# Kernel tuning notes

Hardware: AMD Instinct MI355X
Metric: run time of the kernel (lower is better)

## Reference

```python
import jax, jax.numpy as jnp
import numpy as np

V_SIZES = [2562, 10242, 40962]
E_SIZES = [7680, 30720, 122880]
NG = 8000


def _chamfer(a, b):
    # a: [Na,3], b: [Nb,3] -> squared NN distances (dist_a:[Na], dist_b:[Nb])
    # ||a-b||^2 = ||a||^2 + ||b||^2 - 2 a.b  (GEMM form, same math as pairwise diff)
    an = jnp.sum(a * a, axis=-1)
    bn = jnp.sum(b * b, axis=-1)
    d = an[:, None] + bn[None, :] - 2.0 * (a @ b.T)  # [Na,Nb]
    d = jnp.maximum(d, 0.0)
    return d.min(axis=1), d.min(axis=0)


def _edge_regularization(pred, edges):
    # nn.MSELoss(reduction='none') over endpoint pairs, mean, scaled by coord dim
    diff = pred[edges[:, 0]] - pred[edges[:, 1]]  # [E,3]
    return jnp.mean(diff * diff) * pred.shape[-1]


def _laplace_coord(x, lap_idx):
    # x: [N,3]; lap_idx: [N,10] -> cols 0..7 neighbor idx (-1 pad), col 9 count
    nbr = lap_idx[:, :8]
    valid = nbr >= 0
    idx = jnp.where(valid, nbr, 0)
    v = x[idx]                                  # [N,8,3]
    v = jnp.where(valid[..., None], v, 0.0)
    cnt = lap_idx[:, -1].astype(x.dtype)
    return x - v.sum(axis=1) / cnt[:, None]


def _laplace_regularization(feats, pts, lap_idx):
    lap1 = _laplace_coord(feats, lap_idx)
    lap2 = _laplace_coord(pts, lap_idx)
    d = lap1 - lap2
    return jnp.mean(d * d) * lap1.shape[-1]


def _p2m_loss(pred_pts, pred_feats, gt, edges, lap_idx):
    lap_const = [0.2, 1.0, 1.0]
    chamfer_loss = 0.0
    edge_loss = 0.0
    lap_loss = 0.0
    for i in range(3):
        d1, d2 = _chamfer(gt, pred_pts[i])
        chamfer_loss = chamfer_loss + jnp.mean(d1) + jnp.mean(d2)
        edge_loss = edge_loss + _edge_regularization(pred_pts[i], edges[i])
        lap_loss = lap_loss + lap_const[i] * _laplace_regularization(pred_feats[i], pred_pts[i], lap_idx[i])
    loss = 100.0 * chamfer_loss + 0.1 * edge_loss + 0.3 * lap_loss
    return loss, chamfer_loss, edge_loss, lap_loss


def _make_lap_idx(key, V):
    k1, k2 = jax.random.split(key)
    nbr = jax.random.randint(k1, (V, 8), 0, V)
    mask = jax.random.uniform(k2, (V, 8)) < 0.8
    mask = mask.at[:, 0].set(True)  # at least one valid neighbor
    nbr = jnp.where(mask, nbr, -1)
    cnt = mask.sum(axis=1)
    dummy = jnp.zeros((V, 1), jnp.int32)
    return jnp.concatenate([nbr, dummy, cnt[:, None]], axis=1).astype(jnp.int32)


def setup_inputs() -> dict:
    key = jax.random.key(0)
    ks = jax.random.split(key, 16)
    inp = {}
    for i, V in enumerate(V_SIZES):
        inp[f"pred_pts_{i+1}"] = jax.random.normal(ks[i], (V, 3), dtype=jnp.float32)
        inp[f"pred_feats_{i+1}"] = jax.random.normal(ks[3 + i], (V, 3), dtype=jnp.float32)
        inp[f"edges_{i+1}"] = jax.random.randint(ks[6 + i], (E_SIZES[i], 2), 0, V).astype(jnp.int32)
        inp[f"lap_idx_{i+1}"] = _make_lap_idx(ks[9 + i], V)
    inp["gt_pts"] = jax.random.normal(ks[12], (1, NG, 3), dtype=jnp.float32)
    return inp


def reference(pred_pts_1, pred_pts_2, pred_pts_3,
              pred_feats_1, pred_feats_2, pred_feats_3,
              gt_pts,
              edges_1, edges_2, edges_3,
              lap_idx_1, lap_idx_2, lap_idx_3):
    gt = gt_pts.reshape(-1, 3)
    return _p2m_loss(
        [pred_pts_1, pred_pts_2, pred_pts_3],
        [pred_feats_1, pred_feats_2, pred_feats_3],
        gt,
        [edges_1, edges_2, edges_3],
        [lap_idx_1, lap_idx_2, lap_idx_3],
    )
```

## Files before the change

### kernel.cpp

```cpp
#include <hip/hip_runtime.h>

#define NG 8000
#define V1 2562
#define V2 10242
#define V3 40962
#define E1 7680
#define E2 30720
#define E3 122880
#define NPRED (V1 + V2 + V3)
#define ND1   (3 * NG)
#define NMIN  (ND1 + NPRED)
#define ABATCH 16
#define MAXCHUNK 512

struct PassTab {
    int NA[6], NB[6], h[6], xb[6], chunk[6], ooff[6], base[7];
};

__device__ __forceinline__ double block_reduce_add(double v, double* sm) {
    int lane = threadIdx.x & 63;
    int wid  = threadIdx.x >> 6;
    for (int off = 32; off > 0; off >>= 1) v += __shfl_down(v, off, 64);
    if (lane == 0) sm[wid] = v;
    __syncthreads();
    double r = 0.0;
    if (wid == 0) {
        int nw = blockDim.x >> 6;
        r = (lane < nw) ? sm[lane] : 0.0;
        for (int off = 32; off > 0; off >>= 1) r += __shfl_down(r, off, 64);
    }
    return r;
}

__global__ void k_init(unsigned int* __restrict__ mins, double* __restrict__ acc) {
    int i = blockIdx.x * blockDim.x + threadIdx.x;
    if (i < 8) acc[i] = 0.0;
    int stride = gridDim.x * blockDim.x;
    for (int k = i; k < NMIN; k += stride) mins[k] = 0x7f800000u;
}

__launch_bounds__(256)
__global__ void k_pair_all(const float* __restrict__ gt,
                           const float* __restrict__ q1,
                           const float* __restrict__ q2,
                           const float* __restrict__ q3,
                           unsigned int* __restrict__ mins, PassTab T) {
    __shared__ float4 sb[MAXCHUNK];
    int bid = blockIdx.x, tid = threadIdx.x;

    int p = 0;
    while (p < 5 && bid >= T.base[p + 1]) ++p;
    int rel  = bid - T.base[p];
    int xb   = T.xb[p];
    int xblk = rel % xb, yblk = rel / xb;
    int NA = T.NA[p], NB = T.NB[p], h = T.h[p], chunk = T.chunk[p];
    int pi = (p < 3) ? p : p - 3;
    const float* pr = (pi == 0) ? q1 : ((pi == 1) ? q2 : q3);
    const float* A  = (p < 3) ? gt : pr;
    const float* B  = (p < 3) ? pr : gt;

    int j0 = yblk * chunk;
    int cnt = min(NB - j0, chunk);
    for (int i = tid; i < cnt; i += 256) {
        int j = 3 * (j0 + i);
        float x = B[j], y = B[j + 1], z = B[j + 2];
        sb[i] = make_float4(x, y, z, fmaf(x, x, fmaf(y, y, z * z)));
    }
    __syncthreads();

    int t = xblk * 256 + tid;
    if (t >= h) return;

    float nx[ABATCH], ny_[ABATCH], nz[ABATCH], aw[ABATCH], m[ABATCH];
#pragma unroll
    for (int q = 0; q < ABATCH; ++q) {
        int tq = t + q * h; if (tq > NA - 1) tq = NA - 1;
        int j = 3 * tq;
        float x = A[j], y = A[j + 1], z = A[j + 2];
        nx[q] = -2.f * x; ny_[q] = -2.f * y; nz[q] = -2.f * z;
        aw[q] = fmaf(x, x, fmaf(y, y, z * z));
        m[q] = __builtin_inff();
    }

#define DOT(q, bb) fmaf(nz[q], bb.z, fmaf(ny_[q], bb.y, fmaf(nx[q], bb.x, bb.w)))
    int k = 0;
    for (; k + 2 <= cnt; k += 2) {
        float4 b0 = sb[k], b1 = sb[k + 1];
#pragma unroll
        for (int q = 0; q < ABATCH; ++q) {
            float d0 = DOT(q, b0), d1 = DOT(q, b1);
            m[q] = fminf(fminf(m[q], d0), d1);
        }
    }
    if (k < cnt) {
        float4 b = sb[k];
#pragma unroll
        for (int q = 0; q < ABATCH; ++q) m[q] = fminf(m[q], DOT(q, b));
    }
#undef DOT

    unsigned int* out = mins + T.ooff[p];
#pragma unroll
    for (int q = 0; q < ABATCH; ++q) {
        int tq = t + q * h;
        if (tq < NA) atomicMin(out + tq, __float_as_uint(fmaxf(aw[q] + m[q], 0.f)));
    }
}

#define R0 NMIN
#define R1 (E1 + E2 + E3)
#define R2 NPRED
__global__ void k_post(const unsigned int* __restrict__ mins,
                       const float* __restrict__ p1, const float* __restrict__ p2,
                       const float* __restrict__ p3,
                       const int* __restrict__ e1, const int* __restrict__ e2,
                       const int* __restrict__ e3,
                       const float* __restrict__ f1, const float* __restrict__ f2,
                       const float* __restrict__ f3,
                       const int* __restrict__ l1, const int* __restrict__ l2,
                       const int* __restrict__ l3,
                       double* __restrict__ acc) {
    __shared__ double sm[8];
    double s0 = 0.0, s1 = 0.0, s2 = 0.0;
    int stride = gridDim.x * blockDim.x;
    int gid = blockIdx.x * blockDim.x + threadIdx.x;
    for (int i = gid; i < R0 + R1 + R2; i += stride) {
        if (i < R0) {
            double w;
            if (i < ND1) w = 1.0 / NG;
            else {
                int t = i - ND1;
                w = (t < V1) ? (1.0 / V1) : ((t < V1 + V2) ? (1.0 / V2) : (1.0 / V3));
            }
            s0 += (double)__uint_as_float(mins[i]) * w;
        } else if (i < R0 + R1) {
            int q = i - R0;
            const float* p; const int* e; int k; double w;
            if (q < E1)            { p = p1; e = e1; k = q;            w = 1.0 / E1; }
            else if (q < E1 + E2)  { p = p2; e = e2; k = q - E1;       w = 1.0 / E2; }
            else                   { p = p3; e = e3; k = q - E1 - E2;  w = 1.0 / E3; }
            int u = e[2 * k], v = e[2 * k + 1];
            float dx = p[3 * u]     - p[3 * v];
            float dy = p[3 * u + 1] - p[3 * v + 1];
            float dz = p[3 * u + 2] - p[3 * v + 2];
            s1 += w * (double)(dx * dx + dy * dy + dz * dz);
        } else {
            int q = i - R0 - R1;
            const float* f; const float* p; const int* l; int k; double w;
            if (q < V1)            { f = f1; p = p1; l = l1; k = q;            w = 0.2 / V1; }
            else if (q < V1 + V2)  { f = f2; p = p2; l = l2; k = q - V1;       w = 1.0 / V2; }
            else                   { f = f3; p = p3; l = l3; k = q - V1 - V2;  w = 1.0 / V3; }
            const int* row = l + 10 * k;
            float sfx = 0.f, sfy = 0.f, sfz = 0.f, spx = 0.f, spy = 0.f, spz = 0.f;
#pragma unroll
            for (int r = 0; r < 8; ++r) {
                int n = row[r];
                if (n >= 0) {
                    sfx += f[3 * n]; sfy += f[3 * n + 1]; sfz += f[3 * n + 2];
                    spx += p[3 * n]; spy += p[3 * n + 1]; spz += p[3 * n + 2];
                }
            }
            float inv = 1.0f / (float)row[9];
            float dx = (f[3 * k]     - p[3 * k])     - (sfx - spx) * inv;
            float dy = (f[3 * k + 1] - p[3 * k + 1]) - (sfy - spy) * inv;
            float dz = (f[3 * k + 2] - p[3 * k + 2]) - (sfz - spz) * inv;
            s2 += w * (double)(dx * dx + dy * dy + dz * dz);
        }
    }
    double r0 = block_reduce_add(s0, sm); __syncthreads();
    double r1 = block_reduce_add(s1, sm); __syncthreads();
    double r2 = block_reduce_add(s2, sm);
    if (threadIdx.x == 0) {
        atomicAdd(acc + 0, r0);
        atomicAdd(acc + 1, r1);
        atomicAdd(acc + 2, r2);
    }
}

__global__ void k_final(const double* __restrict__ acc, float* __restrict__ out) {
    if (threadIdx.x == 0 && blockIdx.x == 0) {
        double ch = acc[0], ed = acc[1], lp = acc[2];
        out[0] = (float)(100.0 * ch + 0.1 * ed + 0.3 * lp);
        out[1] = (float)ch;
        out[2] = (float)ed;
        out[3] = (float)lp;
    }
}

static void build_tab(PassTab& T) {
    const int NAs[6]  = { NG, NG, NG, V1, V2, V3 };
    const int NBs[6]  = { V1, V2, V3, NG, NG, NG };
    const int ooff[6] = { 0, NG, 2 * NG, ND1, ND1 + V1, ND1 + V1 + V2 };
    const double totalPairs = 2.0 * ((double)NG * NPRED);
    const int TARGET_BLOCKS = 1024;
    int base = 0;
    for (int p = 0; p < 6; ++p) {
        int NA = NAs[p], NB = NBs[p];
        int h  = (NA + ABATCH - 1) / ABATCH;
        int xb = (h + 255) / 256;
        double share = ((double)NA * NB) / totalPairs;
        int ny = (int)(share * TARGET_BLOCKS / xb + 0.5);
        int nyMin = (NB + MAXCHUNK - 1) / MAXCHUNK;
        int nyMax = NB / 128;
        if (nyMax < nyMin) nyMax = nyMin;
        if (ny < nyMin) ny = nyMin;
        if (ny > nyMax) ny = nyMax;
        int chunk = (NB + ny - 1) / ny;
        ny = (NB + chunk - 1) / chunk;
        T.NA[p] = NA; T.NB[p] = NB; T.h[p] = h; T.xb[p] = xb;
        T.chunk[p] = chunk; T.ooff[p] = ooff[p]; T.base[p] = base;
        base += xb * ny;
    }
    T.base[6] = base;
}

extern "C" void kernel_launch(void* const* d_in, const int* in_sizes, int n_in,
                              void* d_out, int out_size, void* d_ws, size_t ws_size,
                              hipStream_t stream) {
    const float *pp[3], *pf[3], *gt;
    const int *ed[3], *li[3];
    if (in_sizes[1] == 3 * V1) {
        pp[0] = (const float*)d_in[0];  pf[0] = (const float*)d_in[1];
        ed[0] = (const int*)d_in[2];    li[0] = (const int*)d_in[3];
        pp[1] = (const float*)d_in[4];  pf[1] = (const float*)d_in[5];
        ed[1] = (const int*)d_in[6];    li[1] = (const int*)d_in[7];
        pp[2] = (const float*)d_in[8];  pf[2] = (const float*)d_in[9];
        ed[2] = (const int*)d_in[10];   li[2] = (const int*)d_in[11];
        gt = (const float*)d_in[12];
    } else {
        pp[0] = (const float*)d_in[0];  pp[1] = (const float*)d_in[1];  pp[2] = (const float*)d_in[2];
        pf[0] = (const float*)d_in[3];  pf[1] = (const float*)d_in[4];  pf[2] = (const float*)d_in[5];
        gt    = (const float*)d_in[6];
        ed[0] = (const int*)d_in[7];    ed[1] = (const int*)d_in[8];    ed[2] = (const int*)d_in[9];
        li[0] = (const int*)d_in[10];   li[1] = (const int*)d_in[11];   li[2] = (const int*)d_in[12];
    }

    PassTab T;
    build_tab(T);

    char* ws = (char*)d_ws;
    double*       acc  = (double*)ws;
    unsigned int* mins = (unsigned int*)(ws + 64);

    k_init<<<160, 256, 0, stream>>>(mins, acc);
    k_pair_all<<<T.base[6], 256, 0, stream>>>(gt, pp[0], pp[1], pp[2], mins, T);
    k_post<<<256, 256, 0, stream>>>(mins, pp[0], pp[1], pp[2],
                                    ed[0], ed[1], ed[2],
                                    pf[0], pf[1], pf[2],
                                    li[0], li[1], li[2], acc);
    k_final<<<1, 64, 0, stream>>>(acc, (float*)d_out);
}
```

Before: 171.0 us.

## Compute chamfer pairwise distances with bf16 split-precision MFMA matrix ops

```diff
diff --git a/kernel.cpp b/kernel.cpp
--- a/kernel.cpp
+++ b/kernel.cpp
@@ -8,14 +8,34 @@
 #define E2 30720
 #define E3 122880
 #define NPRED (V1 + V2 + V3)
+#define NPK   (NG + NPRED)
 #define ND1   (3 * NG)
 #define NMIN  (ND1 + NPRED)
-#define ABATCH 16
-#define MAXCHUNK 512
-
-struct PassTab {
-    int NA[6], NB[6], h[6], xb[6], chunk[6], ooff[6], base[7];
-};
+#define CHUNK 512
+#define AAW   128
+#define ABLK  512
+
+typedef __attribute__((ext_vector_type(8))) short bf16x8;
+typedef __attribute__((ext_vector_type(4))) float f32x4;
+
+struct PassTab { int NA[6], NB[6], Aoff[6], Boff[6], ooff[6], xb[6], base[7]; };
+
+__device__ __forceinline__ float min3f(float a, float b, float c) {
+    float r;
+    asm("v_min3_f32 %0, %1, %2, %3" : "=v"(r) : "v"(a), "v"(b), "v"(c));
+    return r;
+}
+
+__device__ __forceinline__ unsigned short f2bf(float f) {
+    unsigned int u = __float_as_uint(f);
+    return (unsigned short)((u + 0x7fffu + ((u >> 16) & 1u)) >> 16);
+}
+__device__ __forceinline__ float bf2f(unsigned short b) {
+    return __uint_as_float(((unsigned int)b) << 16);
+}
+__device__ __forceinline__ unsigned int pk(unsigned short lo, unsigned short hi) {
+    return (unsigned int)lo | ((unsigned int)hi << 16);
+}
 
 __device__ __forceinline__ double block_reduce_add(double v, double* sm) {
     int lane = threadIdx.x & 63;
@@ -32,20 +52,52 @@
     return r;
 }
 
-__global__ void k_init(unsigned int* __restrict__ mins, double* __restrict__ acc) {
-    int i = blockIdx.x * blockDim.x + threadIdx.x;
-    if (i < 8) acc[i] = 0.0;
+__global__ void k_prep(const float* __restrict__ gt,
+                       const float* __restrict__ q1, const float* __restrict__ q2,
+                       const float* __restrict__ q3,
+                       uint4* __restrict__ Arec, uint4* __restrict__ Brec,
+                       float* __restrict__ an, unsigned int* __restrict__ mins,
+                       double* __restrict__ acc) {
     int stride = gridDim.x * blockDim.x;
-    for (int k = i; k < NMIN; k += stride) mins[k] = 0x7f800000u;
+    for (int i = blockIdx.x * blockDim.x + threadIdx.x; i < NMIN; i += stride) {
+        if (i < 8) acc[i] = 0.0;
+        mins[i] = 0x7f800000u;
+        if (i < NPK) {
+            const float* src; int k;
+            if (i < NG) { src = gt; k = i; }
+            else {
+                int t = i - NG;
+                if (t < V1)            { src = q1; k = t; }
+                else if (t < V1 + V2)  { src = q2; k = t - V1; }
+                else                   { src = q3; k = t - V1 - V2; }
+            }
+            float x = src[3 * k], y = src[3 * k + 1], z = src[3 * k + 2];
+            unsigned short hx = f2bf(x), hy = f2bf(y), hz = f2bf(z);
+            float hxf = bf2f(hx), hyf = bf2f(hy), hzf = bf2f(hz);
+            unsigned short lx = f2bf(x - hxf), ly = f2bf(y - hyf), lz = f2bf(z - hzf);
+            float bn = fmaf(x, x, fmaf(y, y, z * z));
+            unsigned short bnh = f2bf(bn);
+            unsigned short bnl = f2bf(bn - bf2f(bnh));
+            unsigned short nhx = f2bf(-2.f * hxf), nhy = f2bf(-2.f * hyf), nhz = f2bf(-2.f * hzf);
+            unsigned short nlx = f2bf(-2.f * bf2f(lx)), nly = f2bf(-2.f * bf2f(ly)), nlz = f2bf(-2.f * bf2f(lz));
+            size_t p = (size_t)i;
+            Arec[p * 4 + 0] = make_uint4(pk(nhx, nhy), pk(nhz, nhx), pk(nhy, nhz), pk(0x3F80, 0x3F80));
+            Arec[p * 4 + 1] = make_uint4(pk(nlx, nly), pk(nlz, 0), 0u, 0u);
+            Arec[p * 4 + 2] = make_uint4(0u, 0u, 0u, 0u);
+            Arec[p * 4 + 3] = make_uint4(0u, 0u, 0u, 0u);
+            Brec[p * 2 + 0] = make_uint4(pk(hx, hy), pk(hz, lx), pk(ly, lz), pk(bnh, bnl));
+            Brec[p * 2 + 1] = make_uint4(pk(hx, hy), pk(hz, 0), 0u, 0u);
+            an[i] = bn;
+        }
+    }
 }
 
 __launch_bounds__(256)
-__global__ void k_pair_all(const float* __restrict__ gt,
-                           const float* __restrict__ q1,
-                           const float* __restrict__ q2,
-                           const float* __restrict__ q3,
-                           unsigned int* __restrict__ mins, PassTab T) {
-    __shared__ float4 sb[MAXCHUNK];
+__global__ void k_pair_mfma(const uint4* __restrict__ Arec,
+                            const uint4* __restrict__ Brec,
+                            const float* __restrict__ an,
+                            unsigned int* __restrict__ mins, PassTab T) {
+    __shared__ uint4 sb[2 * CHUNK];
     int bid = blockIdx.x, tid = threadIdx.x;
 
     int p = 0;
@@ -53,57 +105,66 @@
     int rel  = bid - T.base[p];
     int xb   = T.xb[p];
     int xblk = rel % xb, yblk = rel / xb;
-    int NA = T.NA[p], NB = T.NB[p], h = T.h[p], chunk = T.chunk[p];
-    int pi = (p < 3) ? p : p - 3;
-    const float* pr = (pi == 0) ? q1 : ((pi == 1) ? q2 : q3);
-    const float* A  = (p < 3) ? gt : pr;
-    const float* B  = (p < 3) ? pr : gt;
-
-    int j0 = yblk * chunk;
-    int cnt = min(NB - j0, chunk);
-    for (int i = tid; i < cnt; i += 256) {
-        int j = 3 * (j0 + i);
-        float x = B[j], y = B[j + 1], z = B[j + 2];
-        sb[i] = make_float4(x, y, z, fmaf(x, x, fmaf(y, y, z * z)));
+    int NA = T.NA[p], NB = T.NB[p];
+    int Aoff = T.Aoff[p], Boff = T.Boff[p], ooff = T.ooff[p];
+
+    int j0  = yblk * CHUNK;
+    int cnt = min(NB - j0, CHUNK);
+
+    for (int i = tid; i < 2 * CHUNK; i += 256) {
+        int pt = i >> 1, gg = i & 1;
+        uint4 v;
+        if (pt < cnt) v = Brec[(size_t)(Boff + j0 + pt) * 2 + gg];
+        else          v = gg ? make_uint4(0u, 0u, 0u, 0u)
+                             : make_uint4(0u, 0u, 0u, 0x00007F80u);
+        sb[i] = v;
     }
     __syncthreads();
 
-    int t = xblk * 256 + tid;
-    if (t >= h) return;
-
-    float nx[ABATCH], ny_[ABATCH], nz[ABATCH], aw[ABATCH], m[ABATCH];
+    int l = tid & 63, w = tid >> 6;
+    int g = l >> 4, c = l & 15;
+    int Abase = xblk * ABLK + w * AAW;
+
+    union U { uint4 u; bf16x8 b; };
+
+    bf16x8 af[8];
+    float  m[8];
 #pragma unroll
-    for (int q = 0; q < ABATCH; ++q) {
-        int tq = t + q * h; if (tq > NA - 1) tq = NA - 1;
-        int j = 3 * tq;
-        float x = A[j], y = A[j + 1], z = A[j + 2];
-        nx[q] = -2.f * x; ny_[q] = -2.f * y; nz[q] = -2.f * z;
-        aw[q] = fmaf(x, x, fmaf(y, y, z * z));
-        m[q] = __builtin_inff();
-    }
-
-#define DOT(q, bb) fmaf(nz[q], bb.z, fmaf(ny_[q], bb.y, fmaf(nx[q], bb.x, bb.w)))
-    int k = 0;
-    for (; k + 2 <= cnt; k += 2) {
-        float4 b0 = sb[k], b1 = sb[k + 1];
+    for (int tt = 0; tt < 8; ++tt) {
+        int apt = Abase + tt * 16 + c;
+        int ap  = min(apt, NA - 1);
+        U u; u.u = Arec[(size_t)(Aoff + ap) * 4 + g];
+        af[tt] = u.b;
+        m[tt]  = __builtin_inff();
+    }
+
+    unsigned int msk = (g < 2) ? 0xFFFFFFFFu : 0u;
+    const uint4* bbase = sb + (c * 2 + (g & 1));
+    f32x4 zero = {0.f, 0.f, 0.f, 0.f};
+
+    for (int jb = 0; jb < cnt; jb += 16) {
+        uint4 r = bbase[jb * 2];
+        r.x &= msk; r.y &= msk; r.z &= msk; r.w &= msk;
+        U u; u.u = r;
+        bf16x8 bfr = u.b;
 #pragma unroll
-        for (int q = 0; q < ABATCH; ++q) {
-            float d0 = DOT(q, b0), d1 = DOT(q, b1);
-            m[q] = fminf(fminf(m[q], d0), d1);
+        for (int tt = 0; tt < 8; ++tt) {
+            f32x4 a = __builtin_amdgcn_mfma_f32_16x16x32_bf16(bfr, af[tt], zero, 0, 0, 0);
+            float t0 = min3f(a[0], a[1], a[2]);
+            m[tt] = min3f(m[tt], t0, a[3]);
         }
     }
-    if (k < cnt) {
-        float4 b = sb[k];
+
 #pragma unroll
-        for (int q = 0; q < ABATCH; ++q) m[q] = fminf(m[q], DOT(q, b));
-    }
-#undef DOT
-
-    unsigned int* out = mins + T.ooff[p];
-#pragma unroll
-    for (int q = 0; q < ABATCH; ++q) {
-        int tq = t + q * h;
-        if (tq < NA) atomicMin(out + tq, __float_as_uint(fmaxf(aw[q] + m[q], 0.f)));
+    for (int tt = 0; tt < 8; ++tt) {
+        float mm = m[tt];
+        mm = fminf(mm, __shfl_xor(mm, 16, 64));
+        mm = fminf(mm, __shfl_xor(mm, 32, 64));
+        int apt = Abase + tt * 16 + c;
+        if (g == 0 && apt < NA) {
+            float d = fmaxf(an[Aoff + apt] + mm, 0.f);
+            atomicMin(mins + ooff + apt, __float_as_uint(d));
+        }
     }
 }
 
@@ -190,25 +251,16 @@
 static void build_tab(PassTab& T) {
     const int NAs[6]  = { NG, NG, NG, V1, V2, V3 };
     const int NBs[6]  = { V1, V2, V3, NG, NG, NG };
-    const int ooff[6] = { 0, NG, 2 * NG, ND1, ND1 + V1, ND1 + V1 + V2 };
-    const double totalPairs = 2.0 * ((double)NG * NPRED);
-    const int TARGET_BLOCKS = 1024;
+    const int AoP[6]  = { 0, 0, 0, NG, NG + V1, NG + V1 + V2 };
+    const int BoP[6]  = { NG, NG + V1, NG + V1 + V2, 0, 0, 0 };
+    const int ooP[6]  = { 0, NG, 2 * NG, ND1, ND1 + V1, ND1 + V1 + V2 };
     int base = 0;
     for (int p = 0; p < 6; ++p) {
-        int NA = NAs[p], NB = NBs[p];
-        int h  = (NA + ABATCH - 1) / ABATCH;
-        int xb = (h + 255) / 256;
-        double share = ((double)NA * NB) / totalPairs;
-        int ny = (int)(share * TARGET_BLOCKS / xb + 0.5);
-        int nyMin = (NB + MAXCHUNK - 1) / MAXCHUNK;
-        int nyMax = NB / 128;
-        if (nyMax < nyMin) nyMax = nyMin;
-        if (ny < nyMin) ny = nyMin;
-        if (ny > nyMax) ny = nyMax;
-        int chunk = (NB + ny - 1) / ny;
-        ny = (NB + chunk - 1) / chunk;
-        T.NA[p] = NA; T.NB[p] = NB; T.h[p] = h; T.xb[p] = xb;
-        T.chunk[p] = chunk; T.ooff[p] = ooff[p]; T.base[p] = base;
+        int xb = (NAs[p] + ABLK - 1) / ABLK;
+        int ny = (NBs[p] + CHUNK - 1) / CHUNK;
+        T.NA[p] = NAs[p]; T.NB[p] = NBs[p];
+        T.Aoff[p] = AoP[p]; T.Boff[p] = BoP[p]; T.ooff[p] = ooP[p];
+        T.xb[p] = xb; T.base[p] = base;
         base += xb * ny;
     }
     T.base[6] = base;
@@ -240,10 +292,13 @@
 
     char* ws = (char*)d_ws;
     double*       acc  = (double*)ws;
-    unsigned int* mins = (unsigned int*)(ws + 64);
-
-    k_init<<<160, 256, 0, stream>>>(mins, acc);
-    k_pair_all<<<T.base[6], 256, 0, stream>>>(gt, pp[0], pp[1], pp[2], mins, T);
+    unsigned int* mins = (unsigned int*)(ws + 1024);
+    float*        an   = (float*)(ws + 400 * 1024);
+    uint4*        Arec = (uint4*)(ws + 1024 * 1024);
+    uint4*        Brec = (uint4*)(ws + 6 * 1024 * 1024);
+
+    k_prep<<<256, 256, 0, stream>>>(gt, pp[0], pp[1], pp[2], Arec, Brec, an, mins, acc);
+    k_pair_mfma<<<T.base[6], 256, 0, stream>>>(Arec, Brec, an, mins, T);
     k_post<<<256, 256, 0, stream>>>(mins, pp[0], pp[1], pp[2],
                                     ed[0], ed[1], ed[2],
                                     pf[0], pf[1], pf[2],
```

Result: faster. 162.1 us (-5.2%).
